# Optimization experiments

Measured on AMD Instinct MI355X. Metric: run time of the kernel, lower is better.

## Reference

```python
import jax, jax.numpy as jnp
import numpy as np

# ---- module config (from init_kwargs) ----
VOL_RANGE = np.array([-40.0, -40.0, -4.0, 40.0, 40.0, 4.0], np.float32)
VOXEL_SIZE = 0.4
GRID = tuple(int(v) for v in ((VOL_RANGE[3:] - VOL_RANGE[:3]) / VOXEL_SIZE).astype(np.int32))  # (200,200,20)
SIGMA_FACTOR = 3.0
OPACITY_THRESH = 1e-4
EPS = 1e-6
K = 8  # fixed local window per Gaussian (covers 3*sigma_max/voxel_size span)

B, N, C = 1, 25000, 8


def setup_inputs() -> dict:
    key = jax.random.key(0)
    k1, k2, k3, k4, k5 = jax.random.split(key, 5)
    lo = jnp.asarray(VOL_RANGE[:3]) + 1.0
    hi = jnp.asarray(VOL_RANGE[3:]) - 1.0
    means3d = lo + (hi - lo) * jax.random.uniform(k1, (B, N, 3), jnp.float32)
    opacities = jax.random.uniform(k2, (B, N, 1), jnp.float32)
    scales = 0.05 + 0.3 * jax.random.uniform(k3, (B, N, 3), jnp.float32)  # sigma_max=0.35m -> <=6 voxel span
    rotations = jax.random.normal(k4, (B, N, 4), jnp.float32)
    features = jax.random.normal(k5, (B, N, C), jnp.float32)
    return {"means3d": means3d, "opacities": opacities, "scales": scales,
            "rotations": rotations, "features": features}


def quat_scale_to_cov(scales, rotations):
    # matches CUDAVoxelizer._get_covariance
    q = rotations / jnp.sqrt(jnp.sum(rotations ** 2, -1, keepdims=True) + 1e-8)
    r, x, y, z = q[..., 0], q[..., 1], q[..., 2], q[..., 3]
    R = jnp.stack([
        1 - 2 * (y * y + z * z), 2 * (x * y - r * z), 2 * (x * z + r * y),
        2 * (x * y + r * z), 1 - 2 * (x * x + z * z), 2 * (y * z - r * x),
        2 * (x * z - r * y), 2 * (y * z + r * x), 1 - 2 * (x * x + y * y),
    ], axis=-1).reshape(q.shape[:-1] + (3, 3))
    L = R * scales[..., None, :]  # R @ diag(scales)
    return L @ jnp.swapaxes(L, -1, -2)


def voxelize_one(means, opac, cov, feats):
    """means [N,3], opac [N,1], cov [N,3,3], feats [N,C] -> density [X,Y,Z,1], gfeat [X,Y,Z,C]."""
    X, Y, Z = GRID
    V = X * Y * Z
    vol_min = jnp.asarray(VOL_RANGE[:3])
    vol_max = jnp.asarray(VOL_RANGE[3:])
    gmax = jnp.asarray(GRID, jnp.int32) - 1

    sigma = jnp.sqrt(jnp.diagonal(cov, axis1=-2, axis2=-1))          # [N,3]
    bmin = means - SIGMA_FACTOR * sigma
    bmax = means + SIGMA_FACTOR * sigma
    # _filter_gaussians_torch as a multiplicative mask (removed Gaussians contribute 0)
    keep = (jnp.all(bmax > vol_min, -1) & jnp.all(bmin < vol_max, -1)
            & (opac[:, 0] > OPACITY_THRESH))                          # [N]

    cov_inv = jnp.linalg.inv(cov)                                     # [N,3,3]
    bmin_s = jax.lax.stop_gradient(bmin)
    bmax_s = jax.lax.stop_gradient(bmax)
    # torch .int() truncates toward zero; clamp as in fallback
    idx_min = jnp.maximum(((bmin_s - vol_min) / VOXEL_SIZE).astype(jnp.int32), 0)     # [N,3]
    idx_max = jnp.minimum(((bmax_s - vol_min) / VOXEL_SIZE).astype(jnp.int32), gmax)  # [N,3]

    o = jnp.arange(K, dtype=jnp.int32)
    offs = jnp.stack(jnp.meshgrid(o, o, o, indexing='ij'), -1).reshape(-1, 3)  # [P,3], P=K^3
    vox = idx_min[:, None, :] + offs[None]                            # [N,P,3]
    valid = jnp.all(vox <= idx_max[:, None, :], -1)                   # [N,P]

    centers = vox.astype(jnp.float32) * VOXEL_SIZE + vol_min + 0.5 * VOXEL_SIZE
    diff = centers - means[:, None, :]                                # [N,P,3]
    maha = jnp.einsum('npi,nij,npj->np', diff, cov_inv, diff)
    contrib = opac * jnp.exp(-0.5 * maha)                             # [N,P] (opac [N,1] bcast)
    contrib = jnp.where(valid & keep[:, None], contrib, 0.0)

    flat = (vox[..., 0] * Y + vox[..., 1]) * Z + vox[..., 2]
    flat = jnp.clip(flat, 0, V - 1).reshape(-1)                       # zeroed contribs land harmlessly

    density = jnp.zeros((V,), jnp.float32).at[flat].add(contrib.reshape(-1))
    gfeat = jnp.zeros((V, C), jnp.float32).at[flat].add(
        (contrib[..., None] * feats[:, None, :]).reshape(-1, C))
    gfeat = gfeat / jnp.clip(density, EPS)[:, None]
    return density.reshape(X, Y, Z, 1), gfeat.reshape(X, Y, Z, C)


def reference(means3d, opacities, scales, rotations, features):
    cov = quat_scale_to_cov(scales.reshape(-1, 3), rotations.reshape(-1, 4))
    cov = cov.reshape(means3d.shape[0], -1, 3, 3)
    density, gfeat = jax.vmap(voxelize_one)(means3d, opacities, cov, features)
    return density, gfeat
```

## Files before the change

### kernel.cpp

```cpp
#include <hip/hip_runtime.h>

namespace {
constexpr int GX = 200, GY = 200, GZ = 20;
constexpr int NVOX = GX * GY * GZ;
constexpr float VMINX = -40.f, VMINY = -40.f, VMINZ = -4.f;
constexpr float VMAXX =  40.f, VMAXY =  40.f, VMAXZ =  4.f;
constexpr float VS    = 0.4f;
constexpr float HVS   = 0.2f;
constexpr float SIGF  = 3.0f;

constexpr int TILE   = 4;
constexpr int ZSEG   = 4;
constexpr int TX     = GX / TILE;
constexpr int TY     = GY / TILE;
constexpr int TZ     = GZ / ZSEG;
constexpr int NTILES = TX * TY * TZ;
constexpr int CAP    = 128;
constexpr int PSTRIDE = 20;
}

__device__ __forceinline__ bool gauss_setup(
    const float* __restrict__ means, const float* __restrict__ opacs,
    const float* __restrict__ scales, const float* __restrict__ rots,
    int g,
    int& gx0, int& gx1, int& gy0, int& gy1, int& gz0, int& gz1,
    float& i00, float& i01, float& i02, float& i11, float& i12, float& i22,
    float& mx, float& my, float& mz, float& op)
{
    op = opacs[g];
    mx = means[3*g+0]; my = means[3*g+1]; mz = means[3*g+2];
    const float sx = scales[3*g+0], sy = scales[3*g+1], sz = scales[3*g+2];
    const float q0 = rots[4*g+0], q1 = rots[4*g+1], q2 = rots[4*g+2], q3 = rots[4*g+3];

    const float qn = sqrtf(q0*q0 + q1*q1 + q2*q2 + q3*q3 + 1e-8f);
    const float r = q0/qn, x = q1/qn, y = q2/qn, z = q3/qn;

    const float R00 = 1.f - 2.f*(y*y + z*z), R01 = 2.f*(x*y - r*z), R02 = 2.f*(x*z + r*y);
    const float R10 = 2.f*(x*y + r*z), R11 = 1.f - 2.f*(x*x + z*z), R12 = 2.f*(y*z - r*x);
    const float R20 = 2.f*(x*z - r*y), R21 = 2.f*(y*z + r*x), R22 = 1.f - 2.f*(x*x + y*y);

    const float s0 = sx*sx, s1 = sy*sy, s2 = sz*sz;
    const float c00 = R00*R00*s0 + R01*R01*s1 + R02*R02*s2;
    const float c01 = R00*R10*s0 + R01*R11*s1 + R02*R12*s2;
    const float c02 = R00*R20*s0 + R01*R21*s1 + R02*R22*s2;
    const float c11 = R10*R10*s0 + R11*R11*s1 + R12*R12*s2;
    const float c12 = R10*R20*s0 + R11*R21*s1 + R12*R22*s2;
    const float c22 = R20*R20*s0 + R21*R21*s1 + R22*R22*s2;

    const float sgx = SIGF * sqrtf(c00), sgy = SIGF * sqrtf(c11), sgz = SIGF * sqrtf(c22);
    const float bminx = mx - sgx, bminy = my - sgy, bminz = mz - sgz;
    const float bmaxx = mx + sgx, bmaxy = my + sgy, bmaxz = mz + sgz;

    const bool keep = (bmaxx > VMINX) && (bmaxy > VMINY) && (bmaxz > VMINZ)
                   && (bminx < VMAXX) && (bminy < VMAXY) && (bminz < VMAXZ)
                   && (op > 1e-4f);
    if (!keep) return false;

    gx0 = max((int)((bminx - VMINX) / VS), 0);
    gy0 = max((int)((bminy - VMINY) / VS), 0);
    gz0 = max((int)((bminz - VMINZ) / VS), 0);
    gx1 = min((int)((bmaxx - VMINX) / VS), GX - 1);
    gy1 = min((int)((bmaxy - VMINY) / VS), GY - 1);
    gz1 = min((int)((bmaxz - VMINZ) / VS), GZ - 1);
    gx1 = min(gx1, gx0 + 7);
    gy1 = min(gy1, gy0 + 7);
    gz1 = min(gz1, gz0 + 7);
    if (gx1 < gx0 || gy1 < gy0 || gz1 < gz0) return false;

    const float m00 = c11*c22 - c12*c12;
    const float m01 = c02*c12 - c01*c22;
    const float m02 = c01*c12 - c02*c11;
    const float det = c00*m00 + c01*m01 + c02*m02;
    const float id  = 1.f / det;
    i00 = m00*id; i01 = m01*id; i02 = m02*id;
    i11 = (c00*c22 - c02*c02)*id;
    i12 = (c01*c02 - c00*c12)*id;
    i22 = (c00*c11 - c01*c01)*id;
    return true;
}

__global__ __launch_bounds__(64) void voxel_bin(
    const float* __restrict__ means, const float* __restrict__ opacs,
    const float* __restrict__ scales, const float* __restrict__ rots,
    const float* __restrict__ feats,
    int* __restrict__ counts, int* __restrict__ entries,
    float* __restrict__ params, int N)
{
    const int g = blockIdx.x * blockDim.x + threadIdx.x;
    if (g >= N) return;
    int gx0, gx1, gy0, gy1, gz0, gz1;
    float i00,i01,i02,i11,i12,i22, mx,my,mz, op;
    if (!gauss_setup(means, opacs, scales, rots, g,
                     gx0,gx1,gy0,gy1,gz0,gz1, i00,i01,i02,i11,i12,i22, mx,my,mz, op))
        return;

    float* P = params + (size_t)g * PSTRIDE;
    const float4 f0 = *(const float4*)(feats + 8*g);
    const float4 f1 = *(const float4*)(feats + 8*g + 4);
    *(float4*)(P + 0)  = make_float4(i00, i01, i02, i11);
    *(float4*)(P + 4)  = make_float4(i12, i22, mx, my);
    *(float4*)(P + 8)  = make_float4(mz, op,
                                     __int_as_float(gx0 | (gy0<<8) | (gz0<<16)),
                                     __int_as_float(gx1 | (gy1<<8) | (gz1<<16)));
    *(float4*)(P + 12) = f0;
    *(float4*)(P + 16) = f1;

    const int tx0 = gx0 >> 2, tx1 = gx1 >> 2;
    const int ty0 = gy0 >> 2, ty1 = gy1 >> 2;
    const int tz0 = gz0 >> 2, tz1 = gz1 >> 2;
    for (int tx = tx0; tx <= tx1; ++tx)
        for (int ty = ty0; ty <= ty1; ++ty)
            for (int tz = tz0; tz <= tz1; ++tz) {
                const int t = (tx * TY + ty) * TZ + tz;
                const int slot = atomicAdd(&counts[t], 1);
                if (slot < CAP) entries[t * CAP + slot] = g;
            }
}

__global__ __launch_bounds__(64) void voxel_gather(
    const float* __restrict__ params,
    const int* __restrict__ counts, const int* __restrict__ entries,
    float* __restrict__ density, float* __restrict__ gfeat)
{
    const int tile = blockIdx.x;
    const int seg  = tile % TZ;
    const int txy  = tile / TZ;
    const int ttx  = txy / TY, tty = txy % TY;
    const int tid  = threadIdx.x;
    const int cnt  = min(counts[tile], CAP);
    const int base = tile * CAP;

    const int lz = tid & 3, ly = (tid >> 2) & 3, lx = tid >> 4;
    const int vx = ttx * TILE + lx, vy = tty * TILE + ly, vz = seg * ZSEG + lz;
    const float cx = (float)vx * VS + VMINX + HVS;
    const float cy = (float)vy * VS + VMINY + HVS;
    const float cz = (float)vz * VS + VMINZ + HVS;

    float den = 0.f;
    float ft0 = 0.f, ft1 = 0.f, ft2 = 0.f, ft3 = 0.f;
    float ft4 = 0.f, ft5 = 0.f, ft6 = 0.f, ft7 = 0.f;

    for (int j = 0; j < cnt; ++j) {
        const int g = __builtin_amdgcn_readfirstlane(entries[base + j]);
        const float* P = params + (size_t)g * PSTRIDE;

        const int w0 = __float_as_int(P[10]);
        const int w1 = __float_as_int(P[11]);
        const int gx0 = w0 & 255, gy0 = (w0 >> 8) & 255, gz0 = (w0 >> 16) & 255;
        const int gx1 = w1 & 255, gy1 = (w1 >> 8) & 255, gz1 = (w1 >> 16) & 255;
        const bool inw = (vx >= gx0) & (vx <= gx1) & (vy >= gy0) & (vy <= gy1)
                       & (vz >= gz0) & (vz <= gz1);

        const float ddx = cx - P[6], ddy = cy - P[7], ddz = cz - P[8];
        const float maha = P[0]*ddx*ddx + P[3]*ddy*ddy + P[5]*ddz*ddz
                         + 2.f*(P[1]*ddx*ddy + P[2]*ddx*ddz + P[4]*ddy*ddz);
        float w = P[9] * __expf(-0.5f * maha);
        w = inw ? w : 0.f;
        den += w;
        ft0 += w * P[12]; ft1 += w * P[13]; ft2 += w * P[14]; ft3 += w * P[15];
        ft4 += w * P[16]; ft5 += w * P[17]; ft6 += w * P[18]; ft7 += w * P[19];
    }

    const int flat = (vx * GY + vy) * GZ + vz;
    density[flat] = den;
    const float inv = 1.f / fmaxf(den, 1e-6f);
    float4 a = make_float4(ft0*inv, ft1*inv, ft2*inv, ft3*inv);
    float4 b = make_float4(ft4*inv, ft5*inv, ft6*inv, ft7*inv);
    *(float4*)(gfeat + (size_t)flat * 8)     = a;
    *(float4*)(gfeat + (size_t)flat * 8 + 4) = b;
}

extern "C" void kernel_launch(void* const* d_in, const int* in_sizes, int n_in,
                              void* d_out, int out_size, void* d_ws, size_t ws_size,
                              hipStream_t stream)
{
    const float* means  = (const float*)d_in[0];
    const float* opacs  = (const float*)d_in[1];
    const float* scales = (const float*)d_in[2];
    const float* rots   = (const float*)d_in[3];
    const float* feats  = (const float*)d_in[4];

    float* density = (float*)d_out;
    float* gfeat   = density + NVOX;
    const int N = in_sizes[0] / 3;

    int*   counts  = (int*)d_ws;
    int*   entries = counts + NTILES;
    float* params  = (float*)(entries + (size_t)NTILES * CAP);

    hipMemsetAsync(counts, 0, NTILES * sizeof(int), stream);

    voxel_bin<<<(N + 63) / 64, 64, 0, stream>>>(means, opacs, scales, rots, feats,
                                                counts, entries, params, N);
    voxel_gather<<<NTILES, 64, 0, stream>>>(params, counts, entries, density, gfeat);
}
```

Baseline: 114.8 us.

## Store full Gaussian records per tile bin instead of indices

The binning kernel now writes each Gaussian's 20-float parameter record straight into every tile bin it overlaps, rather than storing an index into a shared params array. The gather kernel then reads records contiguously per tile, which removes the dependent index load and the scattered pointer chase, and the loop is unrolled by two. In exchange, write traffic and workspace size grow because each Gaussian's record is duplicated across all the tiles it touches.

```diff
diff --git a/kernel.cpp b/kernel.cpp
--- a/kernel.cpp
+++ b/kernel.cpp
@@ -83,8 +83,7 @@
     const float* __restrict__ means, const float* __restrict__ opacs,
     const float* __restrict__ scales, const float* __restrict__ rots,
     const float* __restrict__ feats,
-    int* __restrict__ counts, int* __restrict__ entries,
-    float* __restrict__ params, int N)
+    int* __restrict__ counts, float* __restrict__ records, int N)
 {
     const int g = blockIdx.x * blockDim.x + threadIdx.x;
     if (g >= N) return;
@@ -94,16 +93,13 @@
                      gx0,gx1,gy0,gy1,gz0,gz1, i00,i01,i02,i11,i12,i22, mx,my,mz, op))
         return;
 
-    float* P = params + (size_t)g * PSTRIDE;
-    const float4 f0 = *(const float4*)(feats + 8*g);
-    const float4 f1 = *(const float4*)(feats + 8*g + 4);
-    *(float4*)(P + 0)  = make_float4(i00, i01, i02, i11);
-    *(float4*)(P + 4)  = make_float4(i12, i22, mx, my);
-    *(float4*)(P + 8)  = make_float4(mz, op,
-                                     __int_as_float(gx0 | (gy0<<8) | (gz0<<16)),
-                                     __int_as_float(gx1 | (gy1<<8) | (gz1<<16)));
-    *(float4*)(P + 12) = f0;
-    *(float4*)(P + 16) = f1;
+    const float4 r0 = make_float4(i00, i01, i02, i11);
+    const float4 r1 = make_float4(i12, i22, mx, my);
+    const float4 r2 = make_float4(mz, op,
+                                  __int_as_float(gx0 | (gy0<<8) | (gz0<<16)),
+                                  __int_as_float(gx1 | (gy1<<8) | (gz1<<16)));
+    const float4 r3 = *(const float4*)(feats + 8*g);
+    const float4 r4 = *(const float4*)(feats + 8*g + 4);
 
     const int tx0 = gx0 >> 2, tx1 = gx1 >> 2;
     const int ty0 = gy0 >> 2, ty1 = gy1 >> 2;
@@ -113,13 +109,20 @@
             for (int tz = tz0; tz <= tz1; ++tz) {
                 const int t = (tx * TY + ty) * TZ + tz;
                 const int slot = atomicAdd(&counts[t], 1);
-                if (slot < CAP) entries[t * CAP + slot] = g;
+                if (slot < CAP) {
+                    float* R = records + ((size_t)t * CAP + slot) * PSTRIDE;
+                    *(float4*)(R + 0)  = r0;
+                    *(float4*)(R + 4)  = r1;
+                    *(float4*)(R + 8)  = r2;
+                    *(float4*)(R + 12) = r3;
+                    *(float4*)(R + 16) = r4;
+                }
             }
 }
 
 __global__ __launch_bounds__(64) void voxel_gather(
-    const float* __restrict__ params,
-    const int* __restrict__ counts, const int* __restrict__ entries,
+    const float* __restrict__ records,
+    const int* __restrict__ counts,
     float* __restrict__ density, float* __restrict__ gfeat)
 {
     const int tile = blockIdx.x;
@@ -128,7 +131,7 @@
     const int ttx  = txy / TY, tty = txy % TY;
     const int tid  = threadIdx.x;
     const int cnt  = min(counts[tile], CAP);
-    const int base = tile * CAP;
+    const float* __restrict__ base = records + (size_t)tile * CAP * PSTRIDE;
 
     const int lz = tid & 3, ly = (tid >> 2) & 3, lx = tid >> 4;
     const int vx = ttx * TILE + lx, vy = tty * TILE + ly, vz = seg * ZSEG + lz;
@@ -140,9 +143,9 @@
     float ft0 = 0.f, ft1 = 0.f, ft2 = 0.f, ft3 = 0.f;
     float ft4 = 0.f, ft5 = 0.f, ft6 = 0.f, ft7 = 0.f;
 
+    #pragma unroll 2
     for (int j = 0; j < cnt; ++j) {
-        const int g = __builtin_amdgcn_readfirstlane(entries[base + j]);
-        const float* P = params + (size_t)g * PSTRIDE;
+        const float* __restrict__ P = base + j * PSTRIDE;
 
         const int w0 = __float_as_int(P[10]);
         const int w1 = __float_as_int(P[11]);
@@ -185,12 +188,11 @@
     const int N = in_sizes[0] / 3;
 
     int*   counts  = (int*)d_ws;
-    int*   entries = counts + NTILES;
-    float* params  = (float*)(entries + (size_t)NTILES * CAP);
+    float* records = (float*)((char*)d_ws + ((NTILES * sizeof(int) + 255) & ~255ull));
 
     hipMemsetAsync(counts, 0, NTILES * sizeof(int), stream);
 
     voxel_bin<<<(N + 63) / 64, 64, 0, stream>>>(means, opacs, scales, rots, feats,
-                                                counts, entries, params, N);
-    voxel_gather<<<NTILES, 64, 0, stream>>>(params, counts, entries, density, gfeat);
+                                                counts, records, N);
+    voxel_gather<<<NTILES, 64, 0, stream>>>(records, counts, density, gfeat);
 }
```

Measured after the change: 125.4 us. 1.09x slower.

## Load Gaussian params cooperatively per lane and broadcast via readlane

Applied to the files above, without the earlier changes.

The gather kernel now has each of the 64 lanes load one Gaussian's parameter record with vector loads, then broadcasts the fields to the wave with readlane, instead of every iteration doing scalar loads of one Gaussian. The per-voxel window test becomes a precomputed 64-bit lane mask per Gaussian. The bin kernel also prescales the inverse covariance by -0.5 and stores log(opacity), so the exponent is one FMA chain with no separate multiply by opacity. This trades serialized memory latency per entry for cheap readlane ops. The log-domain opacity adds a small numerical difference, and a zero opacity cannot occur because such Gaussians are filtered out.

```diff
diff --git a/kernel.cpp b/kernel.cpp
--- a/kernel.cpp
+++ b/kernel.cpp
@@ -24,10 +24,10 @@
     const float* __restrict__ scales, const float* __restrict__ rots,
     int g,
     int& gx0, int& gx1, int& gy0, int& gy1, int& gz0, int& gz1,
-    float& i00, float& i01, float& i02, float& i11, float& i12, float& i22,
-    float& mx, float& my, float& mz, float& op)
-{
-    op = opacs[g];
+    float& c0, float& c1, float& c2, float& c3, float& c4, float& c5,
+    float& mx, float& my, float& mz, float& lop)
+{
+    const float op = opacs[g];
     mx = means[3*g+0]; my = means[3*g+1]; mz = means[3*g+2];
     const float sx = scales[3*g+0], sy = scales[3*g+1], sz = scales[3*g+2];
     const float q0 = rots[4*g+0], q1 = rots[4*g+1], q2 = rots[4*g+2], q3 = rots[4*g+3];
@@ -40,14 +40,14 @@
     const float R20 = 2.f*(x*z - r*y), R21 = 2.f*(y*z + r*x), R22 = 1.f - 2.f*(x*x + y*y);
 
     const float s0 = sx*sx, s1 = sy*sy, s2 = sz*sz;
-    const float c00 = R00*R00*s0 + R01*R01*s1 + R02*R02*s2;
-    const float c01 = R00*R10*s0 + R01*R11*s1 + R02*R12*s2;
-    const float c02 = R00*R20*s0 + R01*R21*s1 + R02*R22*s2;
-    const float c11 = R10*R10*s0 + R11*R11*s1 + R12*R12*s2;
-    const float c12 = R10*R20*s0 + R11*R21*s1 + R12*R22*s2;
-    const float c22 = R20*R20*s0 + R21*R21*s1 + R22*R22*s2;
-
-    const float sgx = SIGF * sqrtf(c00), sgy = SIGF * sqrtf(c11), sgz = SIGF * sqrtf(c22);
+    const float v00 = R00*R00*s0 + R01*R01*s1 + R02*R02*s2;
+    const float v01 = R00*R10*s0 + R01*R11*s1 + R02*R12*s2;
+    const float v02 = R00*R20*s0 + R01*R21*s1 + R02*R22*s2;
+    const float v11 = R10*R10*s0 + R11*R11*s1 + R12*R12*s2;
+    const float v12 = R10*R20*s0 + R11*R21*s1 + R12*R22*s2;
+    const float v22 = R20*R20*s0 + R21*R21*s1 + R22*R22*s2;
+
+    const float sgx = SIGF * sqrtf(v00), sgy = SIGF * sqrtf(v11), sgz = SIGF * sqrtf(v22);
     const float bminx = mx - sgx, bminy = my - sgy, bminz = mz - sgz;
     const float bmaxx = mx + sgx, bmaxy = my + sgy, bmaxz = mz + sgz;
 
@@ -67,15 +67,19 @@
     gz1 = min(gz1, gz0 + 7);
     if (gx1 < gx0 || gy1 < gy0 || gz1 < gz0) return false;
 
-    const float m00 = c11*c22 - c12*c12;
-    const float m01 = c02*c12 - c01*c22;
-    const float m02 = c01*c12 - c02*c11;
-    const float det = c00*m00 + c01*m01 + c02*m02;
+    const float m00 = v11*v22 - v12*v12;
+    const float m01 = v02*v12 - v01*v22;
+    const float m02 = v01*v12 - v02*v11;
+    const float det = v00*m00 + v01*m01 + v02*m02;
     const float id  = 1.f / det;
-    i00 = m00*id; i01 = m01*id; i02 = m02*id;
-    i11 = (c00*c22 - c02*c02)*id;
-    i12 = (c01*c02 - c00*c12)*id;
-    i22 = (c00*c11 - c01*c01)*id;
+    const float i00 = m00*id, i01 = m01*id, i02 = m02*id;
+    const float i11 = (v00*v22 - v02*v02)*id;
+    const float i12 = (v01*v02 - v00*v12)*id;
+    const float i22 = (v00*v11 - v01*v01)*id;
+
+    c0 = -0.5f * i00; c3 = -0.5f * i11; c5 = -0.5f * i22;
+    c1 = -i01; c2 = -i02; c4 = -i12;
+    lop = logf(op);
     return true;
 }
 
@@ -89,21 +93,19 @@
     const int g = blockIdx.x * blockDim.x + threadIdx.x;
     if (g >= N) return;
     int gx0, gx1, gy0, gy1, gz0, gz1;
-    float i00,i01,i02,i11,i12,i22, mx,my,mz, op;
+    float c0,c1,c2,c3,c4,c5, mx,my,mz, lop;
     if (!gauss_setup(means, opacs, scales, rots, g,
-                     gx0,gx1,gy0,gy1,gz0,gz1, i00,i01,i02,i11,i12,i22, mx,my,mz, op))
+                     gx0,gx1,gy0,gy1,gz0,gz1, c0,c1,c2,c3,c4,c5, mx,my,mz, lop))
         return;
 
     float* P = params + (size_t)g * PSTRIDE;
-    const float4 f0 = *(const float4*)(feats + 8*g);
-    const float4 f1 = *(const float4*)(feats + 8*g + 4);
-    *(float4*)(P + 0)  = make_float4(i00, i01, i02, i11);
-    *(float4*)(P + 4)  = make_float4(i12, i22, mx, my);
-    *(float4*)(P + 8)  = make_float4(mz, op,
+    *(float4*)(P + 0)  = make_float4(c0, c1, c2, c3);
+    *(float4*)(P + 4)  = make_float4(c4, c5, mx, my);
+    *(float4*)(P + 8)  = make_float4(mz, lop,
                                      __int_as_float(gx0 | (gy0<<8) | (gz0<<16)),
                                      __int_as_float(gx1 | (gy1<<8) | (gz1<<16)));
-    *(float4*)(P + 12) = f0;
-    *(float4*)(P + 16) = f1;
+    *(float4*)(P + 12) = *(const float4*)(feats + 8*g);
+    *(float4*)(P + 16) = *(const float4*)(feats + 8*g + 4);
 
     const int tx0 = gx0 >> 2, tx1 = gx1 >> 2;
     const int ty0 = gy0 >> 2, ty1 = gy1 >> 2;
@@ -117,6 +119,9 @@
             }
 }
 
+#define RLF(v, j) __int_as_float(__builtin_amdgcn_readlane(__float_as_int(v), (j)))
+#define RLI(v, j) __builtin_amdgcn_readlane((int)(v), (j))
+
 __global__ __launch_bounds__(64) void voxel_gather(
     const float* __restrict__ params,
     const int* __restrict__ counts, const int* __restrict__ entries,
@@ -128,10 +133,11 @@
     const int ttx  = txy / TY, tty = txy % TY;
     const int tid  = threadIdx.x;
     const int cnt  = min(counts[tile], CAP);
-    const int base = tile * CAP;
+    const int lbase = tile * CAP;
 
     const int lz = tid & 3, ly = (tid >> 2) & 3, lx = tid >> 4;
-    const int vx = ttx * TILE + lx, vy = tty * TILE + ly, vz = seg * ZSEG + lz;
+    const int ox = ttx * TILE, oy = tty * TILE, oz = seg * ZSEG;
+    const int vx = ox + lx, vy = oy + ly, vz = oz + lz;
     const float cx = (float)vx * VS + VMINX + HVS;
     const float cy = (float)vy * VS + VMINY + HVS;
     const float cz = (float)vz * VS + VMINZ + HVS;
@@ -140,34 +146,62 @@
     float ft0 = 0.f, ft1 = 0.f, ft2 = 0.f, ft3 = 0.f;
     float ft4 = 0.f, ft5 = 0.f, ft6 = 0.f, ft7 = 0.f;
 
-    for (int j = 0; j < cnt; ++j) {
-        const int g = __builtin_amdgcn_readfirstlane(entries[base + j]);
-        const float* P = params + (size_t)g * PSTRIDE;
-
-        const int w0 = __float_as_int(P[10]);
-        const int w1 = __float_as_int(P[11]);
-        const int gx0 = w0 & 255, gy0 = (w0 >> 8) & 255, gz0 = (w0 >> 16) & 255;
-        const int gx1 = w1 & 255, gy1 = (w1 >> 8) & 255, gz1 = (w1 >> 16) & 255;
-        const bool inw = (vx >= gx0) & (vx <= gx1) & (vy >= gy0) & (vy <= gy1)
-                       & (vz >= gz0) & (vz <= gz1);
-
-        const float ddx = cx - P[6], ddy = cy - P[7], ddz = cz - P[8];
-        const float maha = P[0]*ddx*ddx + P[3]*ddy*ddy + P[5]*ddz*ddz
-                         + 2.f*(P[1]*ddx*ddy + P[2]*ddx*ddz + P[4]*ddy*ddz);
-        float w = P[9] * __expf(-0.5f * maha);
-        w = inw ? w : 0.f;
-        den += w;
-        ft0 += w * P[12]; ft1 += w * P[13]; ft2 += w * P[14]; ft3 += w * P[15];
-        ft4 += w * P[16]; ft5 += w * P[17]; ft6 += w * P[18]; ft7 += w * P[19];
+    for (int chunk = 0; chunk < cnt; chunk += 64) {
+        const int rem = min(cnt - chunk, 64);
+        const int id = entries[lbase + chunk + min(tid, rem - 1)];
+        const float* P = params + (size_t)id * PSTRIDE;
+        const float4 p0 = *(const float4*)(P + 0);
+        const float4 p1 = *(const float4*)(P + 4);
+        const float4 p2 = *(const float4*)(P + 8);
+        const float4 p3 = *(const float4*)(P + 12);
+        const float4 p4 = *(const float4*)(P + 16);
+
+        const int w0 = __float_as_int(p2.z), w1 = __float_as_int(p2.w);
+        const int xlo = max((w0 & 255) - ox, 0),        xhi = min((w1 & 255) - ox, 3);
+        const int ylo = max(((w0 >> 8) & 255) - oy, 0), yhi = min(((w1 >> 8) & 255) - oy, 3);
+        const int zlo = max(((w0 >> 16) & 255) - oz, 0), zhi = min(((w1 >> 16) & 255) - oz, 3);
+        const unsigned xm = (xhi >= xlo) ? ((2u << xhi) - (1u << xlo)) : 0u;
+        const unsigned ym = (yhi >= ylo) ? ((2u << yhi) - (1u << ylo)) : 0u;
+        const unsigned zm = (zhi >= zlo) ? ((2u << zhi) - (1u << zlo)) : 0u;
+        unsigned ypat = 0;
+        #pragma unroll
+        for (int q = 0; q < 4; ++q) if ((ym >> q) & 1) ypat |= zm << (4 * q);
+        unsigned long long hm = 0ull;
+        #pragma unroll
+        for (int q = 0; q < 4; ++q) if ((xm >> q) & 1) hm |= (unsigned long long)ypat << (16 * q);
+        const unsigned hm_lo = (unsigned)hm, hm_hi = (unsigned)(hm >> 32);
+
+        for (int j = 0; j < rem; ++j) {
+            const float a  = RLF(p0.x, j), b  = RLF(p0.y, j);
+            const float c  = RLF(p0.z, j), d  = RLF(p0.w, j);
+            const float e  = RLF(p1.x, j), f  = RLF(p1.y, j);
+            const float mx = RLF(p1.z, j), my = RLF(p1.w, j);
+            const float mz = RLF(p2.x, j), lo = RLF(p2.y, j);
+            const unsigned slo = (unsigned)RLI(hm_lo, j);
+            const unsigned shi = (unsigned)RLI(hm_hi, j);
+            const unsigned long long sm = ((unsigned long long)shi << 32) | slo;
+            const bool in = (sm >> tid) & 1;
+
+            const float ddx = cx - mx, ddy = cy - my, ddz = cz - mz;
+            const float ex = lo + ddx*(a*ddx + b*ddy + c*ddz)
+                                + ddy*(d*ddy + e*ddz) + f*ddz*ddz;
+            float w = __expf(ex);
+            w = in ? w : 0.f;
+            den += w;
+            ft0 += w * RLF(p3.x, j); ft1 += w * RLF(p3.y, j);
+            ft2 += w * RLF(p3.z, j); ft3 += w * RLF(p3.w, j);
+            ft4 += w * RLF(p4.x, j); ft5 += w * RLF(p4.y, j);
+            ft6 += w * RLF(p4.z, j); ft7 += w * RLF(p4.w, j);
+        }
     }
 
     const int flat = (vx * GY + vy) * GZ + vz;
     density[flat] = den;
     const float inv = 1.f / fmaxf(den, 1e-6f);
-    float4 a = make_float4(ft0*inv, ft1*inv, ft2*inv, ft3*inv);
-    float4 b = make_float4(ft4*inv, ft5*inv, ft6*inv, ft7*inv);
-    *(float4*)(gfeat + (size_t)flat * 8)     = a;
-    *(float4*)(gfeat + (size_t)flat * 8 + 4) = b;
+    float4 oa = make_float4(ft0*inv, ft1*inv, ft2*inv, ft3*inv);
+    float4 ob = make_float4(ft4*inv, ft5*inv, ft6*inv, ft7*inv);
+    *(float4*)(gfeat + (size_t)flat * 8)     = oa;
+    *(float4*)(gfeat + (size_t)flat * 8 + 4) = ob;
 }
 
 extern "C" void kernel_launch(void* const* d_in, const int* in_sizes, int n_in,
```

Result: faster. 112.5 us (-2.0%).
